# Optimization experiments

Measured on AMD Instinct MI355X. Metric: run time of the kernel, lower is better.

## Reference

```python
import jax, jax.numpy as jnp
import numpy as np

B, K, D = 8, 4000, 256
H, DQ, DV = 8, 32, 32
WIN, PAD = 200, 50
STEP = WIN - 2 * PAD  # 100
BETA = 0.25


def setup_inputs() -> dict:
    key = jax.random.key(0)
    ks = jax.random.split(key, 14)
    s = 0.02
    return {
        "query": jax.random.normal(ks[0], (B, K, D), jnp.float32),
        "key": jax.random.normal(ks[1], (B, K, D), jnp.float32),
        "value": jax.random.normal(ks[2], (B, K, D), jnp.float32),
        "Wq": jax.random.normal(ks[3], (D, H * DQ), jnp.float32) * s,
        "bq": jax.random.normal(ks[4], (H * DQ,), jnp.float32) * s,
        "Wk": jax.random.normal(ks[5], (D, H * DQ), jnp.float32) * s,
        "bk": jax.random.normal(ks[6], (H * DQ,), jnp.float32) * s,
        "Wv": jax.random.normal(ks[7], (D, H * DV), jnp.float32) * s,
        "bv": jax.random.normal(ks[8], (H * DV,), jnp.float32) * s,
        "Wo": jax.random.normal(ks[9], (H * DV, D), jnp.float32) * s,
        "bo": jax.random.normal(ks[10], (D,), jnp.float32) * s,
    }


def _windows(x, n_win):
    starts = jnp.arange(n_win) * STEP
    idx = starts[:, None] + jnp.arange(WIN)[None, :]
    return x[:, :, idx, :]


def reference(query, key, value, Wq, bq, Wk, bk, Wv, bv, Wo, bo):
    b, k_len, d = query.shape
    pad = lambda t: jnp.pad(t, ((0, 0), (PAD, PAD), (0, 0)), mode='edge')  # replicate pad
    qp, kp, vp = pad(query), pad(key), pad(value)
    kpad = k_len + 2 * PAD
    n_win = (kpad - WIN) // STEP + 1

    def proj(x, Wm, bias, dh):
        y = x @ Wm + bias                       # [B, Kp, H*dh]
        return y.reshape(b, kpad, H, dh).transpose(0, 2, 1, 3)  # [B, H, Kp, dh]

    q = _windows(proj(qp, Wq, bq, DQ), n_win)
    kk = _windows(proj(kp, Wk, bk, DQ), n_win)
    v = _windows(proj(vp, Wv, bv, DV), n_win)

    scores = jnp.einsum('bhnid,bhnjd->bhnij', q, kk) / jnp.sqrt(jnp.float32(WIN))
    dist = jnp.abs(jnp.arange(WIN)[:, None] - jnp.arange(WIN)[None, :]).astype(scores.dtype)
    cauchy = (1.0 / (1.0 + BETA * dist * dist)) * (1.0 - jnp.eye(WIN, dtype=scores.dtype))
    scores = scores * cauchy
    causal = jnp.triu(jnp.ones((WIN, WIN), dtype=bool), k=1)  # attention_size is not None -> causal masking
    scores = jnp.where(causal, -jnp.inf, scores)
    attn = jax.nn.softmax(scores, axis=-1)
    out = jnp.einsum('bhnij,bhnjd->bhnid', attn, v)
    out = out[:, :, :, PAD:WIN - PAD, :].reshape(b, H, k_len, DV)
    out = out.transpose(0, 2, 1, 3).reshape(b, k_len, H * DV)  # heads concatenated, head-major slices
    return out @ Wo + bo
```

## Files before the change

### kernel.cpp

```cpp
#include <hip/hip_runtime.h>


typedef __bf16 bf16_t;
typedef __bf16 bf16x8 __attribute__((ext_vector_type(8)));
typedef float  f32x4  __attribute__((ext_vector_type(4)));

#define MFMA16(a, b, c) __builtin_amdgcn_mfma_f32_16x16x32_bf16((a), (b), (c), 0, 0, 0)

typedef __attribute__((address_space(1))) const unsigned char gas_u8;
typedef __attribute__((address_space(3))) unsigned char las_u8;

static __device__ __forceinline__ void gload16(const void* g, void* l) {
  __builtin_amdgcn_global_load_lds((gas_u8*)g, (las_u8*)l, 16, 0, 0);
}

static __device__ __forceinline__ bf16x8 cvt8(float4 a, float4 b) {
  bf16x8 r;
  r[0] = (bf16_t)a.x; r[1] = (bf16_t)a.y; r[2] = (bf16_t)a.z; r[3] = (bf16_t)a.w;
  r[4] = (bf16_t)b.x; r[5] = (bf16_t)b.y; r[6] = (bf16_t)b.z; r[7] = (bf16_t)b.w;
  return r;
}

static __device__ __forceinline__ unsigned short bbits(bf16_t v) {
  union { bf16_t b; unsigned short u; } c; c.b = v; return c.u;
}

__global__ __launch_bounds__(256)
void prep_weights(const float* __restrict__ Wq, const float* __restrict__ Wk,
                  const float* __restrict__ Wv, const float* __restrict__ Wo,
                  bf16_t* __restrict__ wt) {
  const int mat  = blockIdx.x >> 6;
  const int tile = blockIdx.x & 63;
  const int kt = (tile >> 3) * 32, nt = (tile & 7) * 32;
  const float* W = (mat == 0) ? Wq : (mat == 1) ? Wk : (mat == 2) ? Wv : Wo;
  __shared__ float t[32][33];
  const int tx = threadIdx.x & 31, ty = threadIdx.x >> 5;
#pragma unroll
  for (int i = 0; i < 32; i += 8)
    t[ty + i][tx] = W[(size_t)(kt + ty + i) * 256 + nt + tx];
  __syncthreads();
  bf16_t* dst = wt + (size_t)mat * 65536;
#pragma unroll
  for (int i = 0; i < 32; i += 8)
    dst[(size_t)(nt + ty + i) * 256 + kt + tx] = (bf16_t)t[tx][ty + i];
}

__global__ __launch_bounds__(256)
void proj_gemm(const float* __restrict__ qx, const float* __restrict__ kx,
               const float* __restrict__ vx, const bf16_t* __restrict__ wt,
               const float* __restrict__ bq, const float* __restrict__ bk,
               const float* __restrict__ bv,
               bf16_t* __restrict__ qb, bf16_t* __restrict__ kb,
               bf16_t* __restrict__ vt, int M, float qscale) {
  const int mode = blockIdx.y;
  const float* X    = (mode == 0) ? qx : (mode == 1) ? kx : vx;
  const float* bias = (mode == 0) ? bq : (mode == 1) ? bk : bv;
  const bf16_t* W   = wt + (size_t)mode * 65536;

  __shared__ __align__(16) char lds[8192 + 16384];
  char* ldsA = lds;
  char* ldsB = lds + 8192;

  const int tid  = threadIdx.x;
  const int lane = tid & 63;
  const int w    = tid >> 6;
  const int lo   = lane & 15, hi = lane >> 4;
  const int m0   = blockIdx.x * 64;

  const float* asrc[2];
  char* aldst[2];
#pragma unroll
  for (int j = 0; j < 2; ++j) {
    const int s = (w * 2 + j) * 64 + lane;
    const int row = s >> 3, f = s & 7;
    const int ar = (m0 + row < M) ? (m0 + row) : (M - 1);
    asrc[j]  = X + (size_t)ar * 256 + ((f ^ (row & 7)) << 2);
    aldst[j] = ldsA + (w * 2 + j) * 1024;
  }
  const bf16_t* bsrc[4];
  char* bldst[4];
#pragma unroll
  for (int j = 0; j < 4; ++j) {
    const int s = (w * 4 + j) * 64 + lane;
    bsrc[j]  = W + (size_t)(s >> 2) * 256 + ((s & 3) << 3);
    bldst[j] = ldsB + (w * 4 + j) * 1024;
  }
  int abase[4], bbase[4];
#pragma unroll
  for (int mi = 0; mi < 4; ++mi)
    abase[mi] = (((mi * 16 + lo) << 3) + ((2 * hi) ^ (lo & 7))) << 4;
#pragma unroll
  for (int ni = 0; ni < 4; ++ni)
    bbase[ni] = (w * 64 + ni * 16 + lo) * 64 + hi * 16;

  f32x4 acc[4][4] = {};

  for (int kk = 0; kk < 8; ++kk) {
#pragma unroll
    for (int j = 0; j < 2; ++j) gload16(asrc[j] + kk * 32, aldst[j]);
#pragma unroll
    for (int j = 0; j < 4; ++j) gload16(bsrc[j] + kk * 32, bldst[j]);
    __syncthreads();

    bf16x8 af[4], bfv[4];
#pragma unroll
    for (int mi = 0; mi < 4; ++mi) {
      const float4 v0 = *(const float4*)(ldsA + abase[mi]);
      const float4 v1 = *(const float4*)(ldsA + (abase[mi] ^ 16));
      af[mi] = cvt8(v0, v1);
    }
#pragma unroll
    for (int ni = 0; ni < 4; ++ni)
      bfv[ni] = *(const bf16x8*)(ldsB + bbase[ni]);
#pragma unroll
    for (int mi = 0; mi < 4; ++mi)
#pragma unroll
      for (int ni = 0; ni < 4; ++ni)
        acc[mi][ni] = MFMA16(af[mi], bfv[ni], acc[mi][ni]);
    __syncthreads();
  }

#pragma unroll
  for (int mi = 0; mi < 4; ++mi) {
    const int mb = m0 + mi * 16 + hi * 4;
    if (mb >= M) continue;
#pragma unroll
    for (int ni = 0; ni < 4; ++ni) {
      const int n = w * 64 + ni * 16 + lo;
      const float bia = bias[n];
      if (mode == 0) {
#pragma unroll
        for (int rr = 0; rr < 4; ++rr)
          qb[(size_t)(mb + rr) * 256 + n] = (bf16_t)((acc[mi][ni][rr] + bia) * qscale);
      } else if (mode == 1) {
        const int b = mb / 4000, t = mb - b * 4000;
#pragma unroll
        for (int rr = 0; rr < 4; ++rr)
          kb[((size_t)b * 4064 + t + 50 + rr) * 256 + n] = (bf16_t)(acc[mi][ni][rr] + bia);
      } else {
        const int b = mb / 4000, t = mb - b * 4000;
        const int h = n >> 5, dv = n & 31;
        bf16_t* O = vt + ((size_t)((b * 8 + h) * 32 + dv)) * 4064 + t + 50;
        unsigned short e0 = bbits((bf16_t)(acc[mi][ni][0] + bia));
        unsigned short e1 = bbits((bf16_t)(acc[mi][ni][1] + bia));
        unsigned short e2 = bbits((bf16_t)(acc[mi][ni][2] + bia));
        unsigned short e3 = bbits((bf16_t)(acc[mi][ni][3] + bia));
        unsigned* O32 = (unsigned*)O;
        O32[0] = (unsigned)e0 | ((unsigned)e1 << 16);
        O32[1] = (unsigned)e2 | ((unsigned)e3 << 16);
      }
    }
  }
}

__global__ __launch_bounds__(256)
void out_gemm(const bf16_t* __restrict__ ao, const bf16_t* __restrict__ wt,
              const float* __restrict__ bias, float* __restrict__ Out, int M) {
  __shared__ __align__(16) char lds[4096 + 16384];
  char* ldsA = lds;
  char* ldsB = lds + 4096;

  const int tid  = threadIdx.x;
  const int lane = tid & 63;
  const int w    = tid >> 6;
  const int lo   = lane & 15, hi = lane >> 4;
  const int m0   = blockIdx.x * 64;

  const bf16_t* asrc;
  char* aldst;
  {
    const int s = w * 64 + lane;
    const int row = s >> 2;
    const int ar = (m0 + row < M) ? (m0 + row) : (M - 1);
    asrc  = ao + (size_t)ar * 256 + ((s & 3) << 3);
    aldst = ldsA + w * 1024;
  }
  const bf16_t* bsrc[4];
  char* bldst[4];
#pragma unroll
  for (int j = 0; j < 4; ++j) {
    const int s = (w * 4 + j) * 64 + lane;
    bsrc[j]  = wt + (size_t)(s >> 2) * 256 + ((s & 3) << 3);
    bldst[j] = ldsB + (w * 4 + j) * 1024;
  }
  int abase[4], bbase[4];
#pragma unroll
  for (int mi = 0; mi < 4; ++mi)
    abase[mi] = (mi * 16 + lo) * 64 + hi * 16;
#pragma unroll
  for (int ni = 0; ni < 4; ++ni)
    bbase[ni] = (w * 64 + ni * 16 + lo) * 64 + hi * 16;

  f32x4 acc[4][4] = {};

  for (int kk = 0; kk < 8; ++kk) {
    gload16(asrc + kk * 32, aldst);
#pragma unroll
    for (int j = 0; j < 4; ++j) gload16(bsrc[j] + kk * 32, bldst[j]);
    __syncthreads();

    bf16x8 af[4], bfv[4];
#pragma unroll
    for (int mi = 0; mi < 4; ++mi)
      af[mi] = *(const bf16x8*)(ldsA + abase[mi]);
#pragma unroll
    for (int ni = 0; ni < 4; ++ni)
      bfv[ni] = *(const bf16x8*)(ldsB + bbase[ni]);
#pragma unroll
    for (int mi = 0; mi < 4; ++mi)
#pragma unroll
      for (int ni = 0; ni < 4; ++ni)
        acc[mi][ni] = MFMA16(af[mi], bfv[ni], acc[mi][ni]);
    __syncthreads();
  }

#pragma unroll
  for (int mi = 0; mi < 4; ++mi) {
    const int mb = m0 + mi * 16 + hi * 4;
    if (mb >= M) continue;
#pragma unroll
    for (int ni = 0; ni < 4; ++ni) {
      const int n = w * 64 + ni * 16 + lo;
      const float bia = bias[n];
#pragma unroll
      for (int rr = 0; rr < 4; ++rr)
        Out[(size_t)(mb + rr) * 256 + n] = acc[mi][ni][rr] + bia;
    }
  }
}

__global__ void fill_edges(bf16_t* __restrict__ kb, bf16_t* __restrict__ vt, int nb) {
  const int idx = blockIdx.x * 256 + threadIdx.x;
  const int kcnt = nb * 64 * 256;
  if (idx < kcnt) {
    const int b  = idx >> 14;
    const int pp = (idx >> 8) & 63;
    const int nn = idx & 255;
    const int p  = (pp < 50) ? pp : pp + 4000;
    bf16_t v = (pp < 50) ? kb[((size_t)b * 4064 + 50) * 256 + nn] : (bf16_t)0.f;
    kb[((size_t)b * 4064 + p) * 256 + nn] = v;
  } else {
    const int j  = idx - kcnt;
    const int bh = j >> 11;
    const int dv = (j >> 6) & 31;
    const int pp = j & 63;
    const int p  = (pp < 50) ? pp : pp + 4000;
    bf16_t v = (pp < 50) ? vt[((size_t)bh * 32 + dv) * 4064 + 50] : (bf16_t)0.f;
    vt[((size_t)bh * 32 + dv) * 4064 + p] = v;
  }
}

__global__ __launch_bounds__(448)
void attn_win(const bf16_t* __restrict__ qb, const bf16_t* __restrict__ kb,
              const bf16_t* __restrict__ vt, bf16_t* __restrict__ ao) {
  const int blk = blockIdx.x;
  const int n = blk % 40;
  const int h = (blk / 40) & 7;
  const int b = blk / 320;
  const int wv = threadIdx.x >> 6;
  const int lane = threadIdx.x & 63;
  const int lo = lane & 15, hi = lane >> 4;

  __shared__ __align__(16) bf16_t E[7][16][40];

  const int i0 = 50 + 16 * wv;
  int jtmax = (65 + 16 * wv) >> 4;
  if (jtmax > 9) jtmax = 9;
  const int reach = jtmax * 16 + 16;

  int tq = n * 100 + 16 * wv + lo;
  if (tq > 3999) tq = 3999;
  const bf16x8 qf = *(const bf16x8*)&qb[((size_t)b * 4000 + tq) * 256 + h * 32 + hi * 8];

  const f32x4 zero = {0.f, 0.f, 0.f, 0.f};
  bf16x8 onesf;
#pragma unroll
  for (int u = 0; u < 8; ++u) onesf[u] = (bf16_t)1.0f;

  f32x4 o0 = zero, o1 = zero, sm = zero;
  const size_t vbase = ((size_t)((b * 8 + h) * 32)) * 4064 + n * 100;
  const size_t kbase = ((size_t)(b * 4064 + n * 100)) * 256 + h * 32 + hi * 8;
  const int dbase = i0 + hi * 4 - lo;

#pragma unroll
  for (int kt = 0; kt < 5; ++kt) if (kt * 32 < reach) {
#pragma unroll
    for (int half = 0; half < 2; ++half) {
      const int jt = kt * 2 + half;
      if (jt <= jtmax) {
        const bf16x8 kf = *(const bf16x8*)&kb[kbase + (size_t)(jt * 16 + lo) * 256];
        const f32x4 s = MFMA16(qf, kf, zero);
#pragma unroll
        for (int r = 0; r < 4; ++r) {
          const int d = dbase + r - jt * 16;
          const float df = (float)d;
          float c = __builtin_amdgcn_rcpf(__builtin_fmaf(0.25f * df, df, 1.f));
          c = (d == 0) ? 0.f : c;
          float e = __expf(s[r] * c);
          e = (d < 0) ? 0.f : e;
          E[wv][hi * 4 + r][half * 16 + lo] = (bf16_t)e;
        }
      } else {
#pragma unroll
        for (int r = 0; r < 4; ++r)
          E[wv][hi * 4 + r][half * 16 + lo] = (bf16_t)0.f;
      }
    }
    const bf16x8 pf = *(const bf16x8*)&E[wv][lo][hi * 8];
    const bf16x8 v0 = *(const bf16x8*)&vt[vbase + (size_t)lo * 4064 + kt * 32 + hi * 8];
    const bf16x8 v1 = *(const bf16x8*)&vt[vbase + (size_t)(16 + lo) * 4064 + kt * 32 + hi * 8];
    o0 = MFMA16(pf, v0, o0);
    o1 = MFMA16(pf, v1, o1);
    sm = MFMA16(pf, onesf, sm);
  }

#pragma unroll
  for (int r = 0; r < 4; ++r) {
    const int i = i0 + hi * 4 + r;
    if (i < 150) {
      const float ri = __builtin_amdgcn_rcpf(sm[r]);
      const int t = n * 100 + i - 50;
      bf16_t* op = &ao[((size_t)b * 4000 + t) * 256 + h * 32];
      op[lo]      = (bf16_t)(o0[r] * ri);
      op[16 + lo] = (bf16_t)(o1[r] * ri);
    }
  }
}

extern "C" void kernel_launch(void* const* d_in, const int* in_sizes, int n_in,
                              void* d_out, int out_size, void* d_ws, size_t ws_size,
                              hipStream_t stream) {
  (void)in_sizes; (void)n_in; (void)out_size;
  const float* query = (const float*)d_in[0];
  const float* key   = (const float*)d_in[1];
  const float* value = (const float*)d_in[2];
  const float* Wq = (const float*)d_in[3];
  const float* bq = (const float*)d_in[4];
  const float* Wk = (const float*)d_in[5];
  const float* bk = (const float*)d_in[6];
  const float* Wv = (const float*)d_in[7];
  const float* bv = (const float*)d_in[8];
  const float* Wo = (const float*)d_in[9];
  const float* bo = (const float*)d_in[10];

  int bc = 8;
  while (bc > 1 && 524288ull + (unsigned long long)bc * 8257536ull > (unsigned long long)ws_size)
    bc >>= 1;

  bf16_t* wt = (bf16_t*)d_ws;
  bf16_t* qb = wt + 4 * 65536;
  bf16_t* kb = qb + (size_t)bc * 4000 * 256;
  bf16_t* vt = kb + (size_t)bc * 4064 * 256;
  bf16_t* ao = vt + (size_t)bc * 8 * 32 * 4064;

  prep_weights<<<256, 256, 0, stream>>>(Wq, Wk, Wv, Wo, wt);

  const float qscale = 0.07071067811865475f;

  for (int b0 = 0; b0 < 8; b0 += bc) {
    const int M = bc * 4000;
    const int mblk = (M + 63) / 64;
    const float* qx = query + (size_t)b0 * 4000 * 256;
    const float* kx = key   + (size_t)b0 * 4000 * 256;
    const float* vx = value + (size_t)b0 * 4000 * 256;
    float* ox = (float*)d_out + (size_t)b0 * 4000 * 256;

    proj_gemm<<<dim3(mblk, 3), 256, 0, stream>>>(qx, kx, vx, wt, bq, bk, bv,
                                                 qb, kb, vt, M, qscale);
    fill_edges<<<bc * 128, 256, 0, stream>>>(kb, vt, bc);
    attn_win<<<bc * 320, 448, 0, stream>>>(qb, kb, vt, ao);
    out_gemm<<<dim3(mblk), 256, 0, stream>>>(ao, wt + 3 * 65536, bo, ox, M);
  }
}
```

Before: 94.75 us.

## Double-buffer LDS tiles in projection and output GEMMs to overlap loads with MFMA

Both the input projection GEMM and the output GEMM switch from a single LDS stage to two ping-pong buffers. The next K-slice is issued with global_load_lds before the current slice is computed, and a partial vmcnt wait lets those loads run while the MFMAs execute. The intent is to hide global memory latency behind compute in these short K=256 loops. In exchange each kernel uses twice the LDS, which may lower occupancy, and correctness now depends on hand-written waitcnt counts and raw barriers.

```diff
diff --git a/kernel.cpp b/kernel.cpp
--- a/kernel.cpp
+++ b/kernel.cpp
@@ -57,9 +57,7 @@
   const float* bias = (mode == 0) ? bq : (mode == 1) ? bk : bv;
   const bf16_t* W   = wt + (size_t)mode * 65536;
 
-  __shared__ __align__(16) char lds[8192 + 16384];
-  char* ldsA = lds;
-  char* ldsB = lds + 8192;
+  __shared__ __align__(16) char lds[2 * 24576];
 
   const int tid  = threadIdx.x;
   const int lane = tid & 63;
@@ -68,22 +66,22 @@
   const int m0   = blockIdx.x * 64;
 
   const float* asrc[2];
-  char* aldst[2];
+  int aoff[2];
 #pragma unroll
   for (int j = 0; j < 2; ++j) {
     const int s = (w * 2 + j) * 64 + lane;
     const int row = s >> 3, f = s & 7;
     const int ar = (m0 + row < M) ? (m0 + row) : (M - 1);
-    asrc[j]  = X + (size_t)ar * 256 + ((f ^ (row & 7)) << 2);
-    aldst[j] = ldsA + (w * 2 + j) * 1024;
+    asrc[j] = X + (size_t)ar * 256 + ((f ^ (row & 7)) << 2);
+    aoff[j] = (w * 2 + j) * 1024;
   }
   const bf16_t* bsrc[4];
-  char* bldst[4];
+  int boff[4];
 #pragma unroll
   for (int j = 0; j < 4; ++j) {
     const int s = (w * 4 + j) * 64 + lane;
-    bsrc[j]  = W + (size_t)(s >> 2) * 256 + ((s & 3) << 3);
-    bldst[j] = ldsB + (w * 4 + j) * 1024;
+    bsrc[j] = W + (size_t)(s >> 2) * 256 + ((s & 3) << 3);
+    boff[j] = 8192 + (w * 4 + j) * 1024;
   }
   int abase[4], bbase[4];
 #pragma unroll
@@ -91,33 +89,47 @@
     abase[mi] = (((mi * 16 + lo) << 3) + ((2 * hi) ^ (lo & 7))) << 4;
 #pragma unroll
   for (int ni = 0; ni < 4; ++ni)
-    bbase[ni] = (w * 64 + ni * 16 + lo) * 64 + hi * 16;
+    bbase[ni] = 8192 + (w * 64 + ni * 16 + lo) * 64 + hi * 16;
 
   f32x4 acc[4][4] = {};
 
-  for (int kk = 0; kk < 8; ++kk) {
-#pragma unroll
-    for (int j = 0; j < 2; ++j) gload16(asrc[j] + kk * 32, aldst[j]);
-#pragma unroll
-    for (int j = 0; j < 4; ++j) gload16(bsrc[j] + kk * 32, bldst[j]);
-    __syncthreads();
+#pragma unroll
+  for (int j = 0; j < 2; ++j) gload16(asrc[j], lds + aoff[j]);
+#pragma unroll
+  for (int j = 0; j < 4; ++j) gload16(bsrc[j], lds + boff[j]);
+
+  for (int t = 0; t < 8; ++t) {
+    const int cur = (t & 1) * 24576;
+    if (t < 7) {
+      const int nxt = ((t + 1) & 1) * 24576;
+#pragma unroll
+      for (int j = 0; j < 2; ++j) gload16(asrc[j] + (t + 1) * 32, lds + nxt + aoff[j]);
+#pragma unroll
+      for (int j = 0; j < 4; ++j) gload16(bsrc[j] + (t + 1) * 32, lds + nxt + boff[j]);
+      asm volatile("s_waitcnt vmcnt(6)" ::: "memory");
+    } else {
+      asm volatile("s_waitcnt vmcnt(0)" ::: "memory");
+    }
+    __builtin_amdgcn_sched_barrier(0);
+    __builtin_amdgcn_s_barrier();
 
     bf16x8 af[4], bfv[4];
 #pragma unroll
     for (int mi = 0; mi < 4; ++mi) {
-      const float4 v0 = *(const float4*)(ldsA + abase[mi]);
-      const float4 v1 = *(const float4*)(ldsA + (abase[mi] ^ 16));
+      const float4 v0 = *(const float4*)(lds + cur + abase[mi]);
+      const float4 v1 = *(const float4*)(lds + cur + (abase[mi] ^ 16));
       af[mi] = cvt8(v0, v1);
     }
 #pragma unroll
     for (int ni = 0; ni < 4; ++ni)
-      bfv[ni] = *(const bf16x8*)(ldsB + bbase[ni]);
+      bfv[ni] = *(const bf16x8*)(lds + cur + bbase[ni]);
 #pragma unroll
     for (int mi = 0; mi < 4; ++mi)
 #pragma unroll
       for (int ni = 0; ni < 4; ++ni)
         acc[mi][ni] = MFMA16(af[mi], bfv[ni], acc[mi][ni]);
-    __syncthreads();
+    __builtin_amdgcn_sched_barrier(0);
+    __builtin_amdgcn_s_barrier();
   }
 
 #pragma unroll
@@ -156,9 +168,7 @@
 __global__ __launch_bounds__(256)
 void out_gemm(const bf16_t* __restrict__ ao, const bf16_t* __restrict__ wt,
               const float* __restrict__ bias, float* __restrict__ Out, int M) {
-  __shared__ __align__(16) char lds[4096 + 16384];
-  char* ldsA = lds;
-  char* ldsB = lds + 4096;
+  __shared__ __align__(16) char lds[2 * 20480];
 
   const int tid  = threadIdx.x;
   const int lane = tid & 63;
@@ -167,21 +177,21 @@
   const int m0   = blockIdx.x * 64;
 
   const bf16_t* asrc;
-  char* aldst;
+  int aoff;
   {
     const int s = w * 64 + lane;
     const int row = s >> 2;
     const int ar = (m0 + row < M) ? (m0 + row) : (M - 1);
-    asrc  = ao + (size_t)ar * 256 + ((s & 3) << 3);
-    aldst = ldsA + w * 1024;
+    asrc = ao + (size_t)ar * 256 + ((s & 3) << 3);
+    aoff = w * 1024;
   }
   const bf16_t* bsrc[4];
-  char* bldst[4];
+  int boff[4];
 #pragma unroll
   for (int j = 0; j < 4; ++j) {
     const int s = (w * 4 + j) * 64 + lane;
-    bsrc[j]  = wt + (size_t)(s >> 2) * 256 + ((s & 3) << 3);
-    bldst[j] = ldsB + (w * 4 + j) * 1024;
+    bsrc[j] = wt + (size_t)(s >> 2) * 256 + ((s & 3) << 3);
+    boff[j] = 4096 + (w * 4 + j) * 1024;
   }
   int abase[4], bbase[4];
 #pragma unroll
@@ -189,29 +199,42 @@
     abase[mi] = (mi * 16 + lo) * 64 + hi * 16;
 #pragma unroll
   for (int ni = 0; ni < 4; ++ni)
-    bbase[ni] = (w * 64 + ni * 16 + lo) * 64 + hi * 16;
+    bbase[ni] = 4096 + (w * 64 + ni * 16 + lo) * 64 + hi * 16;
 
   f32x4 acc[4][4] = {};
 
-  for (int kk = 0; kk < 8; ++kk) {
-    gload16(asrc + kk * 32, aldst);
-#pragma unroll
-    for (int j = 0; j < 4; ++j) gload16(bsrc[j] + kk * 32, bldst[j]);
-    __syncthreads();
+  gload16(asrc, lds + aoff);
+#pragma unroll
+  for (int j = 0; j < 4; ++j) gload16(bsrc[j], lds + boff[j]);
+
+  for (int t = 0; t < 8; ++t) {
+    const int cur = (t & 1) * 20480;
+    if (t < 7) {
+      const int nxt = ((t + 1) & 1) * 20480;
+      gload16(asrc + (t + 1) * 32, lds + nxt + aoff);
+#pragma unroll
+      for (int j = 0; j < 4; ++j) gload16(bsrc[j] + (t + 1) * 32, lds + nxt + boff[j]);
+      asm volatile("s_waitcnt vmcnt(5)" ::: "memory");
+    } else {
+      asm volatile("s_waitcnt vmcnt(0)" ::: "memory");
+    }
+    __builtin_amdgcn_sched_barrier(0);
+    __builtin_amdgcn_s_barrier();
 
     bf16x8 af[4], bfv[4];
 #pragma unroll
     for (int mi = 0; mi < 4; ++mi)
-      af[mi] = *(const bf16x8*)(ldsA + abase[mi]);
+      af[mi] = *(const bf16x8*)(lds + cur + abase[mi]);
 #pragma unroll
     for (int ni = 0; ni < 4; ++ni)
-      bfv[ni] = *(const bf16x8*)(ldsB + bbase[ni]);
+      bfv[ni] = *(const bf16x8*)(lds + cur + bbase[ni]);
 #pragma unroll
     for (int mi = 0; mi < 4; ++mi)
 #pragma unroll
       for (int ni = 0; ni < 4; ++ni)
         acc[mi][ni] = MFMA16(af[mi], bfv[ni], acc[mi][ni]);
-    __syncthreads();
+    __builtin_amdgcn_sched_barrier(0);
+    __builtin_amdgcn_s_barrier();
   }
 
 #pragma unroll
```

Result: no change. 94.29 us (-0.5%).
